# Performance work log

Measured on AMD Instinct MI355X. Metric: run time of the kernel, lower is better.

## Reference

```python
import jax, jax.numpy as jnp
import numpy as np

NUM_NODES = 100000
NFEAT = 128
EMBED_DIM = 128
NHEADS = 2
NHID = EMBED_DIM // NHEADS  # 64
REL_DIM = 128
NUM_REL = 500
E1 = 288000  # 1-hop edges
E2 = 32000   # 2-hop edges
E = E1 + E2
ALPHA = 0.2  # LeakyReLU slope
EPS = 1e-16


def setup_inputs() -> dict:
    key = jax.random.key(0)
    ks = jax.random.split(key, 10)
    edge_index = jax.random.randint(ks[0], (2, E), 0, NUM_NODES, dtype=jnp.int32)
    x = jax.random.normal(ks[1], (NUM_NODES, NFEAT), dtype=jnp.float32)
    r = jax.random.normal(ks[2], (NUM_REL, REL_DIM), dtype=jnp.float32)
    edge_type = jax.random.randint(ks[3], (E1,), 0, NUM_REL, dtype=jnp.int32)
    edge_type_nhop = jax.random.randint(ks[4], (E2, 2), 0, NUM_REL, dtype=jnp.int32)
    # learned params (get_param -> xavier-ish normal)
    s = 0.02
    W_heads = jax.random.normal(ks[5], (NHEADS, 2 * NFEAT + REL_DIM, NHID), dtype=jnp.float32) * s
    a_heads = jax.random.normal(ks[6], (NHEADS, NHID, 1), dtype=jnp.float32) * s
    W_out = jax.random.normal(ks[7], (2 * (NHID * NHEADS) + EMBED_DIM, NHEADS * NHID), dtype=jnp.float32) * s
    a_out = jax.random.normal(ks[8], (NHEADS * NHID, 1), dtype=jnp.float32) * s
    W_r = jax.random.normal(ks[9], (REL_DIM, EMBED_DIM), dtype=jnp.float32) * s
    return {"edge_index": edge_index, "x": x, "r": r, "edge_type": edge_type,
            "edge_type_nhop": edge_type_nhop, "W_heads": W_heads, "a_heads": a_heads,
            "W_out": W_out, "a_out": a_out, "W_r": W_r}


def _gat_layer(edge_index, x, edge_embed, W, a, concat):
    src = edge_index[0]
    dst = edge_index[1]
    # [E, 2*in + rel] -> [E, out]
    edge_h = jnp.concatenate([x[src], x[dst], edge_embed], axis=1) @ W
    e = jax.nn.leaky_relu(jnp.squeeze(edge_h @ a, axis=-1), negative_slope=ALPHA)  # [E]
    # segment softmax over src groups
    seg_max = jax.ops.segment_max(e, src, num_segments=NUM_NODES)
    w = jnp.exp(e - seg_max[src])
    denom = jax.ops.segment_sum(w, src, num_segments=NUM_NODES)
    att = w / (denom[src] + EPS)  # dropout p=0.0 -> identity
    out = jax.ops.segment_sum(att[:, None] * edge_h, src, num_segments=NUM_NODES)  # [N, out]
    return jax.nn.elu(out) if concat else out


def reference(edge_index, x, r, edge_type, edge_type_nhop, W_heads, a_heads, W_out, a_out, W_r):
    # first-pass relation edge embeddings
    edge_embed = jnp.concatenate(
        [r[edge_type], r[edge_type_nhop[:, 0]] + r[edge_type_nhop[:, 1]]], axis=0)  # [E, rel]
    # multi-head attention layers (concat heads)
    heads = [_gat_layer(edge_index, x, edge_embed, W_heads[h], a_heads[h], True)
             for h in range(NHEADS)]
    x1 = jnp.concatenate(heads, axis=1)  # [N, nheads*nhid]; dropout p=0 identity
    # transform relations
    r2 = r @ W_r  # [num_rel, embed_dim]
    edge_embed2 = jnp.concatenate(
        [r2[edge_type], r2[edge_type_nhop[:, 0]] + r2[edge_type_nhop[:, 1]]], axis=0)
    out = jax.nn.elu(_gat_layer(edge_index, x1, edge_embed2, W_out, a_out, False))
    return out, r2
```

## Files before the change

### kernel.cpp

```cpp
#include <hip/hip_runtime.h>
#include <math.h>

#define NNODES 100000
#define NREL 500
#define E1 288000
#define ETOT 320000
#define LALPHA 0.2f
#define SEPS 1e-16f
#define NB_SCAN ((NNODES + 255) / 256)
#define GTILES 6250
#define GTPB 5
#define GGRID (GTILES / GTPB)
#define EB 1250

typedef __attribute__((ext_vector_type(8))) short bf16x8;
typedef __attribute__((ext_vector_type(4))) float f32x4;

__device__ __forceinline__ unsigned short f2bf(float x) {
  unsigned int u = __float_as_uint(x);
  unsigned int r = (u + 0x7fffu + ((u >> 16) & 1u)) >> 16;
  return (unsigned short)r;
}
__device__ __forceinline__ unsigned int packbf2(float lo, float hi) {
  return (unsigned int)f2bf(lo) | ((unsigned int)f2bf(hi) << 16);
}
__device__ __forceinline__ float unpk_lo(unsigned int u) { return __uint_as_float(u << 16); }
__device__ __forceinline__ float unpk_hi(unsigned int u) {
  return __uint_as_float(u & 0xffff0000u);
}
__device__ __forceinline__ float lrelu(float e) { return (e >= 0.f) ? e : LALPHA * e; }
__device__ __forceinline__ float wexp(float lg) { return __expf(fminf(lg, 60.f)); }

__device__ __forceinline__ float wave_sum64(float v) {
#pragma unroll
  for (int o = 32; o >= 1; o >>= 1) v += __shfl_xor(v, o, 64);
  return v;
}
__device__ __forceinline__ float red16(float v) {
  v += __shfl_xor(v, 1, 64);
  v += __shfl_xor(v, 2, 64);
  v += __shfl_xor(v, 4, 64);
  v += __shfl_xor(v, 8, 64);
  return v;
}

__global__ void k_zero_int(int* __restrict__ p, int n) {
  int i = blockIdx.x * blockDim.x + threadIdx.x;
  if (i < n) p[i] = 0;
}

__global__ void k_scan_a(const int* __restrict__ cnt, int* __restrict__ rowstart,
                         int* __restrict__ blockTot) {
  __shared__ int s[256];
  int t = threadIdx.x;
  int idx = blockIdx.x * 256 + t;
  int v = (idx < NNODES) ? cnt[idx] : 0;
  s[t] = v;
  __syncthreads();
  for (int off = 1; off < 256; off <<= 1) {
    int xv = (t >= off) ? s[t - off] : 0;
    __syncthreads();
    s[t] += xv;
    __syncthreads();
  }
  if (idx < NNODES) rowstart[idx] = s[t] - v;
  if (t == 255) blockTot[blockIdx.x] = s[255];
}

__global__ void k_scan_b(const int* __restrict__ blockTot, int* __restrict__ blockOff) {
  __shared__ int s[512];
  int t = threadIdx.x;
  int v = (t < NB_SCAN) ? blockTot[t] : 0;
  s[t] = v;
  __syncthreads();
  for (int off = 1; off < 512; off <<= 1) {
    int xv = (t >= off) ? s[t - off] : 0;
    __syncthreads();
    s[t] += xv;
    __syncthreads();
  }
  if (t < NB_SCAN) blockOff[t] = s[t] - v;
}

__global__ void k_scan_c(int* __restrict__ rowstart, const int* __restrict__ blockOff,
                         int* __restrict__ cursor) {
  int idx = blockIdx.x * 256 + threadIdx.x;
  if (idx < NNODES) {
    int v = rowstart[idx] + blockOff[blockIdx.x];
    rowstart[idx] = v;
    cursor[idx] = v;
  }
  if (idx == 0) rowstart[NNODES] = ETOT;
}

#define PREP_GRID (EB + 250 + 250 + 256)
__global__ __launch_bounds__(256) void k_prep(
    const int* __restrict__ srcA, int* __restrict__ cnt, const float* __restrict__ r,
    const float* __restrict__ Wh, const float* __restrict__ ah,
    unsigned int* __restrict__ rW1p, float* __restrict__ srel1,
    const float* __restrict__ Wr, const float* __restrict__ Wo,
    const float* __restrict__ ao, unsigned int* __restrict__ rW2p,
    float* __restrict__ srel2, float* __restrict__ r2out,
    unsigned short* __restrict__ Wb1, unsigned short* __restrict__ Wb2) {
  __shared__ float sm[6 * 128];
  const int b = blockIdx.x;
  const int tid = threadIdx.x;
  if (b < EB) {
    int e = b * 256 + tid;
    if (e < ETOT) atomicAdd(&cnt[srcA[e]], 1);
  } else if (b < EB + 250) {
    float(*vals)[128] = (float(*)[128])sm;
    int rsel = tid >> 7, tid2 = tid & 127;
    int t = (b - EB) * 2 + rsel;
    int h = tid2 >> 6, kk = tid2 & 63;
    const float* wcol = Wh + h * 24576 + 256 * 64 + kk;
    const float* rrow = r + t * 128;
    float acc = 0.f;
#pragma unroll 4
    for (int d = 0; d < 128; ++d) acc = fmaf(rrow[d], wcol[d * 64], acc);
    vals[rsel][tid2] = acc;
    float p = wave_sum64(acc * ah[h * 64 + kk]);
    if (kk == 0) srel1[t * 2 + h] = p;
    __syncthreads();
    if (tid2 < 64) rW1p[t * 64 + tid2] = packbf2(vals[rsel][2 * tid2], vals[rsel][2 * tid2 + 1]);
  } else if (b < EB + 500) {
    float(*v2)[128] = (float(*)[128])sm;
    float(*s)[128] = (float(*)[128])(sm + 2 * 128);
    float(*vals)[128] = (float(*)[128])(sm + 4 * 128);
    int rsel = tid >> 7, k = tid & 127;
    int t = (b - EB - 250) * 2 + rsel;
    float a2 = 0.f;
#pragma unroll 4
    for (int d = 0; d < 128; ++d) a2 = fmaf(r[t * 128 + d], Wr[d * 128 + k], a2);
    r2out[t * 128 + k] = a2;
    v2[rsel][k] = a2;
    __syncthreads();
    float acc = 0.f;
#pragma unroll 4
    for (int d = 0; d < 128; ++d) acc = fmaf(v2[rsel][d], Wo[(256 + d) * 128 + k], acc);
    vals[rsel][k] = acc;
    s[rsel][k] = acc * ao[k];
    __syncthreads();
    for (int off = 64; off >= 1; off >>= 1) {
      if (k < off) s[rsel][k] += s[rsel][k + off];
      __syncthreads();
    }
    if (k == 0) srel2[t] = s[rsel][0];
    if (k < 64) rW2p[t * 64 + k] = packbf2(vals[rsel][2 * k], vals[rsel][2 * k + 1]);
  } else {
    int idx = (b - EB - 500) * 2 + (tid >> 7);
    int layer = idx >> 8, c = idx & 255, d = tid & 127;
    if (layer == 0) {
      int h = (c >> 6) & 1, part = c >> 7, kc = c & 63;
      Wb1[c * 128 + d] = f2bf(Wh[h * 24576 + (part * 128 + d) * 64 + kc]);
    } else {
      int part = c >> 7, kc = c & 127;
      Wb2[c * 128 + d] = f2bf(Wo[(part * 128 + d) * 128 + kc]);
    }
  }
}

template <int LAYER>
__device__ __forceinline__ void gemm_body(int bid, const void* __restrict__ Xin,
                                          const unsigned short* __restrict__ Wb,
                                          const float* __restrict__ avec,
                                          unsigned int* __restrict__ xWp,
                                          float* __restrict__ sc) {
  const int lane = threadIdx.x & 63;
  const int wave = threadIdx.x >> 6;
  const int colv = lane & 15;
  const int kg = lane >> 4;

  bf16x8 b[4][4];
#pragma unroll
  for (int t = 0; t < 4; ++t)
#pragma unroll
    for (int s = 0; s < 4; ++s)
      b[t][s] = *(const bf16x8*)(Wb + (size_t)(wave * 64 + t * 16 + colv) * 128 + s * 32 +
                                 kg * 8);
  float av[4];
#pragma unroll
  for (int t = 0; t < 4; ++t) av[t] = avec[(wave & 1) * 64 + t * 16 + colv];
  const int slot = (LAYER == 1) ? (((wave & 1) << 1) | (wave >> 1)) : wave;

  const float4* xf4 = (const float4*)Xin;
  const uint4* xu4 = (const uint4*)Xin;
  int tile = bid * GTPB;

  float4 cf[8];
  uint4 cu[4];
  {
    int ar = tile * 16 + colv;
    if (LAYER == 1) {
      int base = ar * 32 + kg * 2;
#pragma unroll
      for (int s = 0; s < 4; ++s) {
        cf[2 * s] = xf4[base + s * 8];
        cf[2 * s + 1] = xf4[base + s * 8 + 1];
      }
    } else {
      int base = ar * 16 + kg;
#pragma unroll
      for (int s = 0; s < 4; ++s) cu[s] = xu4[base + s * 4];
    }
  }

  for (int it = 0; it < GTPB; ++it, ++tile) {
    float4 nf[8];
    uint4 nu[4];
    const bool hasnext = (it + 1 < GTPB);
    if (hasnext) {
      int ar = (tile + 1) * 16 + colv;
      if (LAYER == 1) {
        int base = ar * 32 + kg * 2;
#pragma unroll
        for (int s = 0; s < 4; ++s) {
          nf[2 * s] = xf4[base + s * 8];
          nf[2 * s + 1] = xf4[base + s * 8 + 1];
        }
      } else {
        int base = ar * 16 + kg;
#pragma unroll
        for (int s = 0; s < 4; ++s) nu[s] = xu4[base + s * 4];
      }
    }

    bf16x8 a[4];
    if (LAYER == 1) {
#pragma unroll
      for (int s = 0; s < 4; ++s) {
        union {
          unsigned short us[8];
          bf16x8 v;
        } u;
        u.us[0] = f2bf(cf[2 * s].x); u.us[1] = f2bf(cf[2 * s].y);
        u.us[2] = f2bf(cf[2 * s].z); u.us[3] = f2bf(cf[2 * s].w);
        u.us[4] = f2bf(cf[2 * s + 1].x); u.us[5] = f2bf(cf[2 * s + 1].y);
        u.us[6] = f2bf(cf[2 * s + 1].z); u.us[7] = f2bf(cf[2 * s + 1].w);
        a[s] = u.v;
      }
    } else {
#pragma unroll
      for (int s = 0; s < 4; ++s) {
        union {
          uint4 q;
          bf16x8 v;
        } u;
        u.q = cu[s];
        a[s] = u.v;
      }
    }

    f32x4 acc[4];
#pragma unroll
    for (int t = 0; t < 4; ++t) acc[t] = (f32x4){0.f, 0.f, 0.f, 0.f};
#pragma unroll
    for (int s = 0; s < 4; ++s)
#pragma unroll
      for (int t = 0; t < 4; ++t)
        acc[t] = __builtin_amdgcn_mfma_f32_16x16x32_bf16(a[s], b[t][s], acc[t], 0, 0, 0);

    const int rbase = tile * 16 + kg * 4;
    const int m = colv >> 1;
    const bool evn = (colv & 1) == 0;
#pragma unroll
    for (int i = 0; i < 4; ++i) {
      unsigned int* orow = xWp + (size_t)(rbase + i) * 128 + wave * 32;
#pragma unroll
      for (int t = 0; t < 4; ++t) {
        float lo = acc[t][i];
        float other = __shfl_xor(lo, 1, 64);
        if (evn) orow[t * 8 + m] = packbf2(lo, other);
      }
      float p = 0.f;
#pragma unroll
      for (int t = 0; t < 4; ++t) p = fmaf(acc[t][i], av[t], p);
      p = red16(p);
      if (colv == 0) sc[(size_t)(rbase + i) * 4 + slot] = p;
    }

    if (hasnext) {
      if (LAYER == 1) {
#pragma unroll
        for (int j = 0; j < 8; ++j) cf[j] = nf[j];
      } else {
#pragma unroll
        for (int j = 0; j < 4; ++j) cu[j] = nu[j];
      }
    }
  }
}

__global__ __launch_bounds__(256) void k_sg1(
    const int* __restrict__ srcA, const int* __restrict__ dstA, const int* __restrict__ et,
    const int* __restrict__ et2, int* __restrict__ cursor, int* __restrict__ dnp,
    int2* __restrict__ t12, const float* __restrict__ x,
    const unsigned short* __restrict__ Wb1, const float* __restrict__ ah,
    unsigned int* __restrict__ xWp, float* __restrict__ sc1) {
  if (blockIdx.x < EB) {
    int e = blockIdx.x * 256 + threadIdx.x;
    if (e < ETOT) {
      int pos = atomicAdd(&cursor[srcA[e]], 1);
      dnp[pos] = dstA[e];
      int t1, t2 = -1;
      if (e < E1) {
        t1 = et[e];
      } else {
        int2 tt = ((const int2*)et2)[e - E1];
        t1 = tt.x;
        t2 = tt.y;
      }
      t12[pos] = make_int2(t1, t2);
    }
  } else {
    gemm_body<1>(blockIdx.x - EB, x, Wb1, ah, xWp, sc1);
  }
}

__global__ __launch_bounds__(256) void k_gemm2(const void* __restrict__ Xin,
                                               const unsigned short* __restrict__ Wb,
                                               const float* __restrict__ avec,
                                               unsigned int* __restrict__ xWp,
                                               float* __restrict__ sc) {
  gemm_body<2>(blockIdx.x, Xin, Wb, avec, xWp, sc);
}

__global__ __launch_bounds__(256) void k_agg1(
    const int* __restrict__ rowstart, const int* __restrict__ dnp,
    const int2* __restrict__ t12, const unsigned int* __restrict__ xWp,
    const unsigned int* __restrict__ rW1p, const float* __restrict__ sc1,
    const float2* __restrict__ srel1, unsigned int* __restrict__ x1b) {
  int n = blockIdx.x * 4 + (threadIdx.x >> 6);
  int lane = threadIdx.x & 63;
  int q = lane & 15, g = lane >> 4;
  int s0 = rowstart[n];
  int deg = rowstart[n + 1] - s0;
  int jo = 4 * q + g;
  float r0 = 0.f, r1 = 0.f;
  if (deg > 0) {
    float4 scn = ((const float4*)sc1)[n];
    const float ss0 = scn.x, ss1 = scn.z;
    float acL[4] = {0.f, 0.f, 0.f, 0.f}, acH[4] = {0.f, 0.f, 0.f, 0.f};
    float dsum0 = 0.f, dsum1 = 0.f;
    const int pend = s0 + deg;
    for (int p0 = s0; p0 < pend; p0 += 4) {
      int p = p0 + g;
      float w0 = 0.f, w1 = 0.f;
      int dne = 0, t1e = 0, t2e = -1;
      if (p < pend) {
        dne = dnp[p];
        int2 tt = t12[p];
        t1e = tt.x;
        t2e = tt.y;
        float2 sr = srel1[t1e];
        float rel0 = sr.x, rel1 = sr.y;
        if (t2e >= 0) {
          float2 sb = srel1[t2e];
          rel0 += sb.x;
          rel1 += sb.y;
        }
        float4 sdv = ((const float4*)sc1)[dne];
        w0 = wexp(lrelu(ss0 + sdv.y + rel0));
        w1 = wexp(lrelu(ss1 + sdv.w + rel1));
        dsum0 += w0;
        dsum1 += w1;
      }
      uint4 xd = *(const uint4*)(xWp + (size_t)dne * 128 + 64 + 4 * q);
      uint4 rv = *(const uint4*)(rW1p + (size_t)t1e * 64 + 4 * q);
      float rL[4] = {unpk_lo(rv.x), unpk_lo(rv.y), unpk_lo(rv.z), unpk_lo(rv.w)};
      float rH[4] = {unpk_hi(rv.x), unpk_hi(rv.y), unpk_hi(rv.z), unpk_hi(rv.w)};
      if (t2e >= 0) {
        uint4 r2v = *(const uint4*)(rW1p + (size_t)t2e * 64 + 4 * q);
        rL[0] += unpk_lo(r2v.x); rH[0] += unpk_hi(r2v.x);
        rL[1] += unpk_lo(r2v.y); rH[1] += unpk_hi(r2v.y);
        rL[2] += unpk_lo(r2v.z); rH[2] += unpk_hi(r2v.z);
        rL[3] += unpk_lo(r2v.w); rH[3] += unpk_hi(r2v.w);
      }
      float wq = (q < 8) ? w0 : w1;
      acL[0] = fmaf(wq, unpk_lo(xd.x) + rL[0], acL[0]);
      acH[0] = fmaf(wq, unpk_hi(xd.x) + rH[0], acH[0]);
      acL[1] = fmaf(wq, unpk_lo(xd.y) + rL[1], acL[1]);
      acH[1] = fmaf(wq, unpk_hi(xd.y) + rH[1], acH[1]);
      acL[2] = fmaf(wq, unpk_lo(xd.z) + rL[2], acL[2]);
      acH[2] = fmaf(wq, unpk_hi(xd.z) + rH[2], acH[2]);
      acL[3] = fmaf(wq, unpk_lo(xd.w) + rL[3], acL[3]);
      acH[3] = fmaf(wq, unpk_hi(xd.w) + rH[3], acH[3]);
    }
#pragma unroll
    for (int k = 0; k < 4; ++k) {
      acL[k] += __shfl_xor(acL[k], 16, 64);
      acL[k] += __shfl_xor(acL[k], 32, 64);
      acH[k] += __shfl_xor(acH[k], 16, 64);
      acH[k] += __shfl_xor(acH[k], 32, 64);
    }
    dsum0 += __shfl_xor(dsum0, 16, 64);
    dsum0 += __shfl_xor(dsum0, 32, 64);
    dsum1 += __shfl_xor(dsum1, 16, 64);
    dsum1 += __shfl_xor(dsum1, 32, 64);
    float aL = (g == 0) ? acL[0] : (g == 1) ? acL[1] : (g == 2) ? acL[2] : acL[3];
    float aH = (g == 0) ? acH[0] : (g == 1) ? acH[1] : (g == 2) ? acH[2] : acH[3];
    float dsel = (q < 8) ? dsum0 : dsum1;
    float isel = 1.f / (dsel + SEPS);
    unsigned int us = xWp[(size_t)n * 128 + jo];
    float o0 = (aL + dsel * unpk_lo(us)) * isel;
    float o1 = (aH + dsel * unpk_hi(us)) * isel;
    r0 = (o0 > 0.f) ? o0 : __expf(o0) - 1.f;
    r1 = (o1 > 0.f) ? o1 : __expf(o1) - 1.f;
  }
  x1b[(size_t)n * 64 + jo] = packbf2(r0, r1);
}

__global__ __launch_bounds__(256) void k_agg2(
    const int* __restrict__ rowstart, const int* __restrict__ dnp,
    const int2* __restrict__ t12, const unsigned int* __restrict__ xWp,
    const unsigned int* __restrict__ rW2p, const float* __restrict__ sc2,
    const float* __restrict__ srel2, float* __restrict__ outp) {
  int n = blockIdx.x * 4 + (threadIdx.x >> 6);
  int lane = threadIdx.x & 63;
  int q = lane & 15, g = lane >> 4;
  int s0 = rowstart[n];
  int deg = rowstart[n + 1] - s0;
  int jo = 4 * q + g;
  float r0 = 0.f, r1 = 0.f;
  if (deg > 0) {
    float4 scn = ((const float4*)sc2)[n];
    const float ss = scn.x + scn.y;
    float acL[4] = {0.f, 0.f, 0.f, 0.f}, acH[4] = {0.f, 0.f, 0.f, 0.f};
    float dsum = 0.f;
    const int pend = s0 + deg;
    for (int p0 = s0; p0 < pend; p0 += 4) {
      int p = p0 + g;
      float w = 0.f;
      int dne = 0, t1e = 0, t2e = -1;
      if (p < pend) {
        dne = dnp[p];
        int2 tt = t12[p];
        t1e = tt.x;
        t2e = tt.y;
        float rel = srel2[t1e];
        if (t2e >= 0) rel += srel2[t2e];
        float4 sdv = ((const float4*)sc2)[dne];
        w = wexp(lrelu(ss + (sdv.z + sdv.w) + rel));
        dsum += w;
      }
      uint4 xd = *(const uint4*)(xWp + (size_t)dne * 128 + 64 + 4 * q);
      uint4 rv = *(const uint4*)(rW2p + (size_t)t1e * 64 + 4 * q);
      float rL[4] = {unpk_lo(rv.x), unpk_lo(rv.y), unpk_lo(rv.z), unpk_lo(rv.w)};
      float rH[4] = {unpk_hi(rv.x), unpk_hi(rv.y), unpk_hi(rv.z), unpk_hi(rv.w)};
      if (t2e >= 0) {
        uint4 r2v = *(const uint4*)(rW2p + (size_t)t2e * 64 + 4 * q);
        rL[0] += unpk_lo(r2v.x); rH[0] += unpk_hi(r2v.x);
        rL[1] += unpk_lo(r2v.y); rH[1] += unpk_hi(r2v.y);
        rL[2] += unpk_lo(r2v.z); rH[2] += unpk_hi(r2v.z);
        rL[3] += unpk_lo(r2v.w); rH[3] += unpk_hi(r2v.w);
      }
      acL[0] = fmaf(w, unpk_lo(xd.x) + rL[0], acL[0]);
      acH[0] = fmaf(w, unpk_hi(xd.x) + rH[0], acH[0]);
      acL[1] = fmaf(w, unpk_lo(xd.y) + rL[1], acL[1]);
      acH[1] = fmaf(w, unpk_hi(xd.y) + rH[1], acH[1]);
      acL[2] = fmaf(w, unpk_lo(xd.z) + rL[2], acL[2]);
      acH[2] = fmaf(w, unpk_hi(xd.z) + rH[2], acH[2]);
      acL[3] = fmaf(w, unpk_lo(xd.w) + rL[3], acL[3]);
      acH[3] = fmaf(w, unpk_hi(xd.w) + rH[3], acH[3]);
    }
#pragma unroll
    for (int k = 0; k < 4; ++k) {
      acL[k] += __shfl_xor(acL[k], 16, 64);
      acL[k] += __shfl_xor(acL[k], 32, 64);
      acH[k] += __shfl_xor(acH[k], 16, 64);
      acH[k] += __shfl_xor(acH[k], 32, 64);
    }
    dsum += __shfl_xor(dsum, 16, 64);
    dsum += __shfl_xor(dsum, 32, 64);
    float aL = (g == 0) ? acL[0] : (g == 1) ? acL[1] : (g == 2) ? acL[2] : acL[3];
    float aH = (g == 0) ? acH[0] : (g == 1) ? acH[1] : (g == 2) ? acH[2] : acH[3];
    float inv = 1.f / (dsum + SEPS);
    unsigned int us = xWp[(size_t)n * 128 + jo];
    float o0 = (aL + dsum * unpk_lo(us)) * inv;
    float o1 = (aH + dsum * unpk_hi(us)) * inv;
    r0 = (o0 > 0.f) ? o0 : __expf(o0) - 1.f;
    r1 = (o1 > 0.f) ? o1 : __expf(o1) - 1.f;
  }
  ((float2*)outp)[(size_t)n * 64 + jo] = make_float2(r0, r1);
}

extern "C" void kernel_launch(void* const* d_in, const int* in_sizes, int n_in, void* d_out,
                              int out_size, void* d_ws, size_t ws_size, hipStream_t stream) {
  const int* edge_index = (const int*)d_in[0];
  const int* srcA = edge_index;
  const int* dstA = edge_index + ETOT;
  const float* x = (const float*)d_in[1];
  const float* r = (const float*)d_in[2];
  const int* et = (const int*)d_in[3];
  const int* et2 = (const int*)d_in[4];
  const float* Wh = (const float*)d_in[5];
  const float* ah = (const float*)d_in[6];
  const float* Wo = (const float*)d_in[7];
  const float* ao = (const float*)d_in[8];
  const float* Wr = (const float*)d_in[9];
  float* out = (float*)d_out;
  float* r2out = out + (size_t)NNODES * 128;

  char* ws = (char*)d_ws;
  size_t o = 0;
  auto alloc = [&](size_t bytes) {
    char* p = ws + o;
    o += (bytes + 255) & ~(size_t)255;
    return p;
  };
  unsigned int* xWp = (unsigned int*)alloc((size_t)NNODES * 128 * 4);
  float* sc1 = (float*)alloc((size_t)NNODES * 4 * 4);
  float* sc2 = (float*)alloc((size_t)NNODES * 4 * 4);
  unsigned int* rW1p = (unsigned int*)alloc((size_t)NREL * 64 * 4);
  float* srel1 = (float*)alloc(2 * NREL * 4);
  unsigned int* rW2p = (unsigned int*)alloc((size_t)NREL * 64 * 4);
  float* srel2 = (float*)alloc(NREL * 4);
  unsigned int* x1b = (unsigned int*)alloc((size_t)NNODES * 64 * 4);
  unsigned short* Wb1 = (unsigned short*)alloc(256 * 128 * 2);
  unsigned short* Wb2 = (unsigned short*)alloc(256 * 128 * 2);
  int* cnt = (int*)alloc(NNODES * 4);
  int* rowstart = (int*)alloc((NNODES + 1) * 4);
  int* cursor = (int*)alloc(NNODES * 4);
  int* blockTot = (int*)alloc(512 * 4);
  int* blockOff = (int*)alloc(512 * 4);
  int* dnp = (int*)alloc(ETOT * 4);
  int2* t12 = (int2*)alloc((size_t)ETOT * 8);

  k_zero_int<<<(NNODES + 255) / 256, 256, 0, stream>>>(cnt, NNODES);
  k_prep<<<PREP_GRID, 256, 0, stream>>>(srcA, cnt, r, Wh, ah, rW1p, srel1, Wr, Wo, ao, rW2p,
                                        srel2, r2out, Wb1, Wb2);
  k_scan_a<<<NB_SCAN, 256, 0, stream>>>(cnt, rowstart, blockTot);
  k_scan_b<<<1, 512, 0, stream>>>(blockTot, blockOff);
  k_scan_c<<<NB_SCAN, 256, 0, stream>>>(rowstart, blockOff, cursor);
  k_sg1<<<EB + GGRID, 256, 0, stream>>>(srcA, dstA, et, et2, cursor, dnp, t12, x, Wb1, ah,
                                        xWp, sc1);
  k_agg1<<<NNODES / 4, 256, 0, stream>>>(rowstart, dnp, t12, xWp, rW1p, sc1,
                                         (const float2*)srel1, x1b);
  k_gemm2<<<GGRID, 256, 0, stream>>>(x1b, Wb2, ao, xWp, sc2);
  k_agg2<<<NNODES / 4, 256, 0, stream>>>(rowstart, dnp, t12, xWp, rW2p, sc2, srel2, out);
}
```

Before: 348.7 us.

## Pack edge payload into int4, fold scan_b into scan_c, interleave scatter/GEMM blocks

Merges the separate dst-index and type-pair arrays into one 16-byte per-edge record, so each aggregation edge needs a single vector load and the scatter does one store. It also removes the single-block scan_b kernel: each scan_c block now sums the preceding block totals itself with a wave reduction, saving one launch. The scatter and GEMM blocks in k_sg1 are interleaved by even/odd block index so both run concurrently across the grid. The cost is a padded 16-byte record, larger than the previous 12 bytes per edge, and redundant reads of block totals in every scan_c block.

```diff
diff --git a/kernel.cpp b/kernel.cpp
--- a/kernel.cpp
+++ b/kernel.cpp
@@ -32,6 +32,11 @@
 __device__ __forceinline__ float wexp(float lg) { return __expf(fminf(lg, 60.f)); }
 
 __device__ __forceinline__ float wave_sum64(float v) {
+#pragma unroll
+  for (int o = 32; o >= 1; o >>= 1) v += __shfl_xor(v, o, 64);
+  return v;
+}
+__device__ __forceinline__ int wave_sum64i(int v) {
 #pragma unroll
   for (int o = 32; o >= 1; o >>= 1) v += __shfl_xor(v, o, 64);
   return v;
@@ -67,28 +72,24 @@
   if (t == 255) blockTot[blockIdx.x] = s[255];
 }
 
-__global__ void k_scan_b(const int* __restrict__ blockTot, int* __restrict__ blockOff) {
-  __shared__ int s[512];
+__global__ void k_scan_c(int* __restrict__ rowstart, const int* __restrict__ blockTot,
+                         int* __restrict__ cursor) {
+  __shared__ int wred[4];
   int t = threadIdx.x;
-  int v = (t < NB_SCAN) ? blockTot[t] : 0;
-  s[t] = v;
+  int bid = blockIdx.x;
+  int v = 0;
+  if (t < bid) v += blockTot[t];
+  int t2 = t + 256;
+  if (t2 < bid) v += blockTot[t2];
+  v = wave_sum64i(v);
+  if ((t & 63) == 0) wred[t >> 6] = v;
   __syncthreads();
-  for (int off = 1; off < 512; off <<= 1) {
-    int xv = (t >= off) ? s[t - off] : 0;
-    __syncthreads();
-    s[t] += xv;
-    __syncthreads();
-  }
-  if (t < NB_SCAN) blockOff[t] = s[t] - v;
-}
-
-__global__ void k_scan_c(int* __restrict__ rowstart, const int* __restrict__ blockOff,
-                         int* __restrict__ cursor) {
-  int idx = blockIdx.x * 256 + threadIdx.x;
+  int off = wred[0] + wred[1] + wred[2] + wred[3];
+  int idx = bid * 256 + t;
   if (idx < NNODES) {
-    int v = rowstart[idx] + blockOff[blockIdx.x];
-    rowstart[idx] = v;
-    cursor[idx] = v;
+    int val = rowstart[idx] + off;
+    rowstart[idx] = val;
+    cursor[idx] = val;
   }
   if (idx == 0) rowstart[NNODES] = ETOT;
 }
@@ -293,15 +294,15 @@
 
 __global__ __launch_bounds__(256) void k_sg1(
     const int* __restrict__ srcA, const int* __restrict__ dstA, const int* __restrict__ et,
-    const int* __restrict__ et2, int* __restrict__ cursor, int* __restrict__ dnp,
-    int2* __restrict__ t12, const float* __restrict__ x,
-    const unsigned short* __restrict__ Wb1, const float* __restrict__ ah,
-    unsigned int* __restrict__ xWp, float* __restrict__ sc1) {
-  if (blockIdx.x < EB) {
-    int e = blockIdx.x * 256 + threadIdx.x;
+    const int* __restrict__ et2, int* __restrict__ cursor, int4* __restrict__ epay,
+    const float* __restrict__ x, const unsigned short* __restrict__ Wb1,
+    const float* __restrict__ ah, unsigned int* __restrict__ xWp,
+    float* __restrict__ sc1) {
+  const int bid = blockIdx.x;
+  if ((bid & 1) == 0) {
+    int e = (bid >> 1) * 256 + threadIdx.x;
     if (e < ETOT) {
       int pos = atomicAdd(&cursor[srcA[e]], 1);
-      dnp[pos] = dstA[e];
       int t1, t2 = -1;
       if (e < E1) {
         t1 = et[e];
@@ -310,10 +311,10 @@
         t1 = tt.x;
         t2 = tt.y;
       }
-      t12[pos] = make_int2(t1, t2);
+      epay[pos] = make_int4(dstA[e], t1, t2, 0);
     }
   } else {
-    gemm_body<1>(blockIdx.x - EB, x, Wb1, ah, xWp, sc1);
+    gemm_body<1>(bid >> 1, x, Wb1, ah, xWp, sc1);
   }
 }
 
@@ -326,10 +327,10 @@
 }
 
 __global__ __launch_bounds__(256) void k_agg1(
-    const int* __restrict__ rowstart, const int* __restrict__ dnp,
-    const int2* __restrict__ t12, const unsigned int* __restrict__ xWp,
-    const unsigned int* __restrict__ rW1p, const float* __restrict__ sc1,
-    const float2* __restrict__ srel1, unsigned int* __restrict__ x1b) {
+    const int* __restrict__ rowstart, const int4* __restrict__ epay,
+    const unsigned int* __restrict__ xWp, const unsigned int* __restrict__ rW1p,
+    const float* __restrict__ sc1, const float2* __restrict__ srel1,
+    unsigned int* __restrict__ x1b) {
   int n = blockIdx.x * 4 + (threadIdx.x >> 6);
   int lane = threadIdx.x & 63;
   int q = lane & 15, g = lane >> 4;
@@ -348,10 +349,10 @@
       float w0 = 0.f, w1 = 0.f;
       int dne = 0, t1e = 0, t2e = -1;
       if (p < pend) {
-        dne = dnp[p];
-        int2 tt = t12[p];
-        t1e = tt.x;
-        t2e = tt.y;
+        int4 ep = epay[p];
+        dne = ep.x;
+        t1e = ep.y;
+        t2e = ep.z;
         float2 sr = srel1[t1e];
         float rel0 = sr.x, rel1 = sr.y;
         if (t2e >= 0) {
@@ -411,10 +412,10 @@
 }
 
 __global__ __launch_bounds__(256) void k_agg2(
-    const int* __restrict__ rowstart, const int* __restrict__ dnp,
-    const int2* __restrict__ t12, const unsigned int* __restrict__ xWp,
-    const unsigned int* __restrict__ rW2p, const float* __restrict__ sc2,
-    const float* __restrict__ srel2, float* __restrict__ outp) {
+    const int* __restrict__ rowstart, const int4* __restrict__ epay,
+    const unsigned int* __restrict__ xWp, const unsigned int* __restrict__ rW2p,
+    const float* __restrict__ sc2, const float* __restrict__ srel2,
+    float* __restrict__ outp) {
   int n = blockIdx.x * 4 + (threadIdx.x >> 6);
   int lane = threadIdx.x & 63;
   int q = lane & 15, g = lane >> 4;
@@ -433,10 +434,10 @@
       float w = 0.f;
       int dne = 0, t1e = 0, t2e = -1;
       if (p < pend) {
-        dne = dnp[p];
-        int2 tt = t12[p];
-        t1e = tt.x;
-        t2e = tt.y;
+        int4 ep = epay[p];
+        dne = ep.x;
+        t1e = ep.y;
+        t2e = ep.z;
         float rel = srel2[t1e];
         if (t2e >= 0) rel += srel2[t2e];
         float4 sdv = ((const float4*)sc2)[dne];
@@ -522,20 +523,16 @@
   int* rowstart = (int*)alloc((NNODES + 1) * 4);
   int* cursor = (int*)alloc(NNODES * 4);
   int* blockTot = (int*)alloc(512 * 4);
-  int* blockOff = (int*)alloc(512 * 4);
-  int* dnp = (int*)alloc(ETOT * 4);
-  int2* t12 = (int2*)alloc((size_t)ETOT * 8);
+  int4* epay = (int4*)alloc((size_t)ETOT * 16);
 
   k_zero_int<<<(NNODES + 255) / 256, 256, 0, stream>>>(cnt, NNODES);
   k_prep<<<PREP_GRID, 256, 0, stream>>>(srcA, cnt, r, Wh, ah, rW1p, srel1, Wr, Wo, ao, rW2p,
                                         srel2, r2out, Wb1, Wb2);
   k_scan_a<<<NB_SCAN, 256, 0, stream>>>(cnt, rowstart, blockTot);
-  k_scan_b<<<1, 512, 0, stream>>>(blockTot, blockOff);
-  k_scan_c<<<NB_SCAN, 256, 0, stream>>>(rowstart, blockOff, cursor);
-  k_sg1<<<EB + GGRID, 256, 0, stream>>>(srcA, dstA, et, et2, cursor, dnp, t12, x, Wb1, ah,
-                                        xWp, sc1);
-  k_agg1<<<NNODES / 4, 256, 0, stream>>>(rowstart, dnp, t12, xWp, rW1p, sc1,
+  k_scan_c<<<NB_SCAN, 256, 0, stream>>>(rowstart, blockTot, cursor);
+  k_sg1<<<2 * EB, 256, 0, stream>>>(srcA, dstA, et, et2, cursor, epay, x, Wb1, ah, xWp, sc1);
+  k_agg1<<<NNODES / 4, 256, 0, stream>>>(rowstart, epay, xWp, rW1p, sc1,
                                          (const float2*)srel1, x1b);
   k_gemm2<<<GGRID, 256, 0, stream>>>(x1b, Wb2, ao, xWp, sc2);
-  k_agg2<<<NNODES / 4, 256, 0, stream>>>(rowstart, dnp, t12, xWp, rW2p, sc2, srel2, out);
-}
+  k_agg2<<<NNODES / 4, 256, 0, stream>>>(rowstart, epay, xWp, rW2p, sc2, srel2, out);
+}
```

New measurement: 356.6 us. +2.3%, slower.
